# Optimization experiments

Hardware: AMD Instinct MI355X
Metric: run time of the kernel (lower is better)

The kernel has to match this reference:

```python
import jax, jax.numpy as jnp
import numpy as np

TEMPERATURE = 0.1   # g.temperature
THRESHOLD = 0.05    # g.init_threshold
B, LEN_S, LEN_E = 8, 50, 10   # batch, sentence positions, max_word_length
N = B * LEN_S * LEN_E         # number of candidate spans
VOCAB = 30000


def setup_inputs() -> dict:
    key = jax.random.key(0)
    k0, k1 = jax.random.split(key)
    # positive edit-distance-like scores between every candidate span and every vocab word
    ed_dist = jax.random.uniform(k0, (N, VOCAB), dtype=jnp.float32) * 10.0
    flat = jnp.arange(N, dtype=jnp.int64)
    bi = flat // (LEN_S * LEN_E)          # batch index of each candidate
    lsi = (flat // LEN_E) % LEN_S         # start index
    lei = flat % LEN_E                    # (length-1) index
    viable = jax.random.uniform(k1, (N,)) < 0.5
    return {"ed_dist": ed_dist, "bi": bi, "lsi": lsi, "lei": lei, "viable": viable}


def _soft_min(x, axis):
    # w = (-x / T).log_softmax().exp(); value = (x * w).sum; index = argmin
    w = jax.nn.softmax(-x / TEMPERATURE, axis=axis)
    return (x * w).sum(axis), jnp.argmin(x, axis=axis)


def _soft_max(x, axis):
    w = jax.nn.softmax(x / TEMPERATURE, axis=axis)
    return (x * w).sum(axis), jnp.argmax(x, axis=axis)


def _celu(x):  # alpha = 1
    return jnp.where(x > 0, x, jnp.expm1(jnp.minimum(x, 0.0)))


def _soft_threshold(x, thresh):
    return (_celu(1.0 - 2.0 * x / thresh) + 1.0) / 2.0


def _restore_shape(tensor, bi, lsi, lei, viable, value):
    # scatter viable candidates into dense (B, LEN_S, LEN_E); non-viable go to a dump slot
    flat_idx = bi * (LEN_S * LEN_E) + lsi * LEN_E + lei
    dump = B * LEN_S * LEN_E
    idx = jnp.where(viable, flat_idx, dump)
    ret = jnp.full((dump + 1,), value, dtype=tensor.dtype)
    ret = ret.at[idx].set(tensor)
    return ret[:-1].reshape(B, LEN_S, LEN_E)


def reference(ed_dist, bi, lsi, lei, viable):
    # soft-min over vocab: best matched edit distance + hard vocab index
    matched_ed, matched_vocab = _soft_min(ed_dist, axis=-1)
    # soft thresholding to matching score
    matched_thresh = _soft_threshold(matched_ed, THRESHOLD)
    # restore dense (batch, len_s, len_e) shape
    score_dense = _restore_shape(matched_thresh, bi, lsi, lei, viable, 0.0)
    vocab_dense = _restore_shape(matched_vocab, bi, lsi, lei, viable, jnp.array(-1, matched_vocab.dtype))
    # soft-max over all spans per batch element
    flat_scores = score_dense.reshape(B, LEN_S * LEN_E)
    best_matched_score, best_idx = _soft_max(flat_scores, axis=-1)
    best_matched_vocab = jnp.take_along_axis(
        vocab_dense.reshape(B, LEN_S * LEN_E), best_idx[:, None], axis=1)[:, 0]
    start = best_idx // LEN_E
    end = start + best_idx % LEN_E
    return best_matched_score, start, end, best_matched_vocab, score_dense
```

## Files before the change

kernel.cpp:

```cpp
#include <hip/hip_runtime.h>
#include <stdint.h>

#define NROWS 4000
#define NCOLS 30000
#define NC8   3750
#define BATCH 8
#define SPANS 500
#define LEN_E_ 10
#define KLOG2E 14.4269504088896340736f

__device__ __forceinline__ float fexp2(float x) {
    return __builtin_amdgcn_exp2f(x);
}

__device__ __forceinline__ int detect_elem_bytes(const uint8_t* __restrict__ p,
                                                 int tid) {
    __shared__ int s_count;
    if (tid == 0) s_count = 0;
    __syncthreads();
    int c = 0;
#pragma unroll
    for (int k = 0; k < 8; ++k) c += (p[tid * 8 + k] != 0);
#pragma unroll
    for (int off = 32; off > 0; off >>= 1) c += __shfl_down(c, off);
    if ((tid & 63) == 0) atomicAdd(&s_count, c);
    __syncthreads();
    int cnt = s_count;
    return cnt >= 800 ? 1 : (cnt >= 192 ? 4 : 8);
}

__device__ __forceinline__ bool viable_at(const void* __restrict__ p, int esz,
                                          int i) {
    if (esz == 1) return ((const uint8_t*)p)[i] != 0;
    if (esz == 4) return ((const uint32_t*)p)[i] != 0u;
    return ((const unsigned long long*)p)[i] != 0ull;
}

__global__ __launch_bounds__(256) void softmin_rows(
    const float* __restrict__ ed, const void* __restrict__ viable,
    float* __restrict__ out) {
    const int row = blockIdx.x;
    const int tid = threadIdx.x;

    const int esz = detect_elem_bytes((const uint8_t*)viable, tid);

    const float4* __restrict__ rp =
        (const float4*)(ed + (size_t)row * NCOLS);

    float Z = 0.f, S = 0.f;
    for (int j = tid; j < NC8; j += 256) {
        float4 a = rp[2 * j];
        float4 b = rp[2 * j + 1];
#pragma unroll
        for (int c = 0; c < 4; ++c) {
            float x = (&a.x)[c];
            float e = fexp2(x * -KLOG2E);
            Z += e;
            S = fmaf(x, e, S);
        }
#pragma unroll
        for (int c = 0; c < 4; ++c) {
            float x = (&b.x)[c];
            float e = fexp2(x * -KLOG2E);
            Z += e;
            S = fmaf(x, e, S);
        }
    }

#pragma unroll
    for (int off = 32; off > 0; off >>= 1) {
        Z += __shfl_down(Z, off);
        S += __shfl_down(S, off);
    }
    __shared__ float wZ[4], wS[4];
    if ((tid & 63) == 0) { wZ[tid >> 6] = Z; wS[tid >> 6] = S; }
    __syncthreads();

    if (tid == 0) {
        float Zt = (wZ[0] + wZ[1]) + (wZ[2] + wZ[3]);
        float St = (wS[0] + wS[1]) + (wS[2] + wS[3]);
        float ed_v  = St / Zt;
        float z     = 1.f - 40.f * ed_v;
        float celu  = z > 0.f ? z : expm1f(z);
        float score = 0.5f * (celu + 1.f);
        out[32 + row] = viable_at(viable, esz, row) ? score : 0.f;
    }
}

__global__ __launch_bounds__(256) void span_softmax(
    const float* __restrict__ ed, float* __restrict__ out) {
    const int b   = blockIdx.x;
    const int tid = threadIdx.x;
    const float* __restrict__ sc = out + 32 + b * SPANS;

    __shared__ float sv[256];
    __shared__ int   si[256];

    float mx = -INFINITY; int ai = 0;
    for (int j = tid; j < SPANS; j += 256) {
        float x = sc[j];
        if (x > mx) { mx = x; ai = j; }
    }
    sv[tid] = mx; si[tid] = ai;
    __syncthreads();
    for (int off = 128; off > 0; off >>= 1) {
        if (tid < off) {
            float v2 = sv[tid+off]; int i2 = si[tid+off];
            if (v2 > sv[tid] || (v2 == sv[tid] && i2 < si[tid])) {
                sv[tid] = v2; si[tid] = i2;
            }
        }
        __syncthreads();
    }
    const float M    = sv[0];
    const int   best = si[0];
    __syncthreads();

    float Z = 0.f, S = 0.f;
    for (int j = tid; j < SPANS; j += 256) {
        float x = sc[j];
        float e = fexp2((x - M) * KLOG2E);
        Z += e;
        S = fmaf(x, e, S);
    }
    __shared__ float sZ[256], sS[256];
    sZ[tid] = Z; sS[tid] = S;
    __syncthreads();
    for (int off = 128; off > 0; off >>= 1) {
        if (tid < off) { sZ[tid] += sZ[tid+off]; sS[tid] += sS[tid+off]; }
        __syncthreads();
    }
    const float best_score = sS[0] / sZ[0];
    __syncthreads();

    const float4* __restrict__ rp = (const float4*)(
        ed + ((size_t)b * SPANS + (size_t)best) * NCOLS);
    float mv = INFINITY; int vi = 0;
    for (int j = tid; j < NCOLS / 4; j += 256) {
        float4 v = rp[j];
        const int base = j * 4;
#pragma unroll
        for (int c = 0; c < 4; ++c) {
            float x = (&v.x)[c];
            if (x < mv) { mv = x; vi = base + c; }
        }
    }
    sv[tid] = mv; si[tid] = vi;
    __syncthreads();
    for (int off = 128; off > 0; off >>= 1) {
        if (tid < off) {
            float v2 = sv[tid+off]; int i2 = si[tid+off];
            if (v2 < sv[tid] || (v2 == sv[tid] && i2 < si[tid])) {
                sv[tid] = v2; si[tid] = i2;
            }
        }
        __syncthreads();
    }

    if (tid == 0) {
        int start = best / LEN_E_;
        int len   = best % LEN_E_;
        out[b]          = best_score;
        out[8 + b]      = (float)start;
        out[16 + b]     = (float)(start + len);
        out[24 + b]     = (M > 0.f) ? (float)si[0] : -1.f;
    }
}

extern "C" void kernel_launch(void* const* d_in, const int* in_sizes, int n_in,
                              void* d_out, int out_size, void* d_ws,
                              size_t ws_size, hipStream_t stream) {
    const float* ed     = (const float*)d_in[0];
    const void*  viable = d_in[4];
    float* out = (float*)d_out;

    hipLaunchKernelGGL(softmin_rows, dim3(NROWS), dim3(256), 0, stream,
                       ed, viable, out);
    hipLaunchKernelGGL(span_softmax, dim3(BATCH), dim3(256), 0, stream,
                       ed, out);
}
```

Baseline: 106.2 us.

## Compute per-row argmin in softmin pass, drop re-read of best row

The first kernel now tracks a running argmin alongside the softmin sums and writes each row's argmin index to workspace. The second kernel looks up that index for the chosen span instead of re-scanning the 30000-element row with only 8 blocks. The main loop also widens to four float4 loads per iteration. This adds compare/select work per element to the memory-bound pass, in exchange for removing a serial, low-parallelism tail scan.

```diff
diff --git a/kernel.cpp b/kernel.cpp
--- a/kernel.cpp
+++ b/kernel.cpp
@@ -3,7 +3,7 @@
 
 #define NROWS 4000
 #define NCOLS 30000
-#define NC8   3750
+#define NQ4   1875
 #define BATCH 8
 #define SPANS 500
 #define LEN_E_ 10
@@ -38,7 +38,7 @@
 
 __global__ __launch_bounds__(256) void softmin_rows(
     const float* __restrict__ ed, const void* __restrict__ viable,
-    float* __restrict__ out) {
+    float* __restrict__ out, int* __restrict__ amin) {
     const int row = blockIdx.x;
     const int tid = threadIdx.x;
 
@@ -47,23 +47,28 @@
     const float4* __restrict__ rp =
         (const float4*)(ed + (size_t)row * NCOLS);
 
-    float Z = 0.f, S = 0.f;
-    for (int j = tid; j < NC8; j += 256) {
-        float4 a = rp[2 * j];
-        float4 b = rp[2 * j + 1];
+    float Z = 0.f, S = 0.f, mv = INFINITY;
+    int   vi = 0;
+
+    for (int j = tid; j < NQ4; j += 256) {
+        float4 vv[4];
+        vv[0] = rp[4 * j + 0];
+        vv[1] = rp[4 * j + 1];
+        vv[2] = rp[4 * j + 2];
+        vv[3] = rp[4 * j + 3];
+        const int base = j << 4;
 #pragma unroll
-        for (int c = 0; c < 4; ++c) {
-            float x = (&a.x)[c];
-            float e = fexp2(x * -KLOG2E);
-            Z += e;
-            S = fmaf(x, e, S);
-        }
+        for (int q = 0; q < 4; ++q) {
 #pragma unroll
-        for (int c = 0; c < 4; ++c) {
-            float x = (&b.x)[c];
-            float e = fexp2(x * -KLOG2E);
-            Z += e;
-            S = fmaf(x, e, S);
+            for (int c = 0; c < 4; ++c) {
+                float x = (&vv[q].x)[c];
+                float e = fexp2(x * -KLOG2E);
+                Z += e;
+                S = fmaf(x, e, S);
+                bool lt = x < mv;
+                mv = lt ? x : mv;
+                vi = lt ? (base + q * 4 + c) : vi;
+            }
         }
     }
 
@@ -71,24 +76,37 @@
     for (int off = 32; off > 0; off >>= 1) {
         Z += __shfl_down(Z, off);
         S += __shfl_down(S, off);
+        float ov = __shfl_down(mv, off);
+        int   oi = __shfl_down(vi, off);
+        if (ov < mv || (ov == mv && oi < vi)) { mv = ov; vi = oi; }
     }
-    __shared__ float wZ[4], wS[4];
-    if ((tid & 63) == 0) { wZ[tid >> 6] = Z; wS[tid >> 6] = S; }
+    __shared__ float wZ[4], wS[4], wM[4];
+    __shared__ int   wI[4];
+    if ((tid & 63) == 0) {
+        int w = tid >> 6;
+        wZ[w] = Z; wS[w] = S; wM[w] = mv; wI[w] = vi;
+    }
     __syncthreads();
 
     if (tid == 0) {
-        float Zt = (wZ[0] + wZ[1]) + (wZ[2] + wZ[3]);
-        float St = (wS[0] + wS[1]) + (wS[2] + wS[3]);
+        float Zt = 0.f, St = 0.f, m = INFINITY;
+        int ii = 0;
+#pragma unroll
+        for (int w = 0; w < 4; ++w) {
+            Zt += wZ[w]; St += wS[w];
+            if (wM[w] < m || (wM[w] == m && wI[w] < ii)) { m = wM[w]; ii = wI[w]; }
+        }
         float ed_v  = St / Zt;
         float z     = 1.f - 40.f * ed_v;
         float celu  = z > 0.f ? z : expm1f(z);
         float score = 0.5f * (celu + 1.f);
+        amin[row]     = ii;
         out[32 + row] = viable_at(viable, esz, row) ? score : 0.f;
     }
 }
 
 __global__ __launch_bounds__(256) void span_softmax(
-    const float* __restrict__ ed, float* __restrict__ out) {
+    const int* __restrict__ amin, float* __restrict__ out) {
     const int b   = blockIdx.x;
     const int tid = threadIdx.x;
     const float* __restrict__ sc = out + 32 + b * SPANS;
@@ -130,40 +148,14 @@
         if (tid < off) { sZ[tid] += sZ[tid+off]; sS[tid] += sS[tid+off]; }
         __syncthreads();
     }
-    const float best_score = sS[0] / sZ[0];
-    __syncthreads();
-
-    const float4* __restrict__ rp = (const float4*)(
-        ed + ((size_t)b * SPANS + (size_t)best) * NCOLS);
-    float mv = INFINITY; int vi = 0;
-    for (int j = tid; j < NCOLS / 4; j += 256) {
-        float4 v = rp[j];
-        const int base = j * 4;
-#pragma unroll
-        for (int c = 0; c < 4; ++c) {
-            float x = (&v.x)[c];
-            if (x < mv) { mv = x; vi = base + c; }
-        }
-    }
-    sv[tid] = mv; si[tid] = vi;
-    __syncthreads();
-    for (int off = 128; off > 0; off >>= 1) {
-        if (tid < off) {
-            float v2 = sv[tid+off]; int i2 = si[tid+off];
-            if (v2 < sv[tid] || (v2 == sv[tid] && i2 < si[tid])) {
-                sv[tid] = v2; si[tid] = i2;
-            }
-        }
-        __syncthreads();
-    }
 
     if (tid == 0) {
         int start = best / LEN_E_;
         int len   = best % LEN_E_;
-        out[b]          = best_score;
-        out[8 + b]      = (float)start;
-        out[16 + b]     = (float)(start + len);
-        out[24 + b]     = (M > 0.f) ? (float)si[0] : -1.f;
+        out[b]      = sS[0] / sZ[0];
+        out[8 + b]  = (float)start;
+        out[16 + b] = (float)(start + len);
+        out[24 + b] = (M > 0.f) ? (float)amin[b * SPANS + best] : -1.f;
     }
 }
 
@@ -172,10 +164,11 @@
                               size_t ws_size, hipStream_t stream) {
     const float* ed     = (const float*)d_in[0];
     const void*  viable = d_in[4];
-    float* out = (float*)d_out;
+    float* out  = (float*)d_out;
+    int*   amin = (int*)d_ws;
 
     hipLaunchKernelGGL(softmin_rows, dim3(NROWS), dim3(256), 0, stream,
-                       ed, viable, out);
+                       ed, viable, out, amin);
     hipLaunchKernelGGL(span_softmax, dim3(BATCH), dim3(256), 0, stream,
-                       ed, out);
+                       amin, out);
 }
```

Result: faster. 91.43 us (-13.9%).
